# Kernel tuning notes

Measured on AMD Instinct MI355X. Metric: run time of the kernel, lower is better.

The kernel has to match this reference:

```python
import jax, jax.numpy as jnp
import numpy as np

B, T, F = 256, 192, 8
CARD0, CARD1 = 1000, 100
E0, E1 = 32, 16
H = 512
D_IN = F + E0 + E1  # 56


def _glorot(key, shape):
    fan_in, fan_out = shape[0], shape[-1]
    lim = jnp.sqrt(6.0 / (fan_in + fan_out))
    return jax.random.uniform(key, shape, jnp.float32, -lim, lim)


def setup_inputs() -> dict:
    key = jax.random.key(0)
    ks = jax.random.split(key, 16)
    return {
        "x_cont": jax.random.normal(ks[0], (B, T, F), jnp.float32),
        "cat0": jax.random.randint(ks[1], (B, T), 0, CARD0),
        "cat1": jax.random.randint(ks[2], (B, T), 0, CARD1),
        "emb0": _glorot(ks[3], (CARD0, E0)),
        "emb1": _glorot(ks[4], (CARD1, E1)),
        "Wk1": _glorot(ks[5], (D_IN, 4 * H)),
        "Wr1": _glorot(ks[6], (H, 4 * H)),
        "b1": jnp.zeros((4 * H,), jnp.float32).at[H:2 * H].set(1.0),  # unit_forget_bias
        "Wk2": _glorot(ks[7], (H, 4 * H)),
        "Wr2": _glorot(ks[8], (H, 4 * H)),
        "b2": jnp.zeros((4 * H,), jnp.float32).at[H:2 * H].set(1.0),
        "Wmu": _glorot(ks[9], (H, 1)),
        "bmu": _glorot(ks[10], (1, 1))[0],
        "Wsig": _glorot(ks[11], (H, 1)),
        "bsig": _glorot(ks[12], (1, 1))[0],
    }


def _lstm(x, Wk, Wr, b):
    # x: [B, T, D]; Keras gate order i, f, g(c), o; zero initial states (inference mode,
    # dropout/recurrent_dropout inactive when training=False).
    xz = jnp.einsum('btd,dk->btk', x, Wk) + b  # precompute input projection for all steps
    h0 = jnp.zeros((x.shape[0], H), x.dtype)

    def step(carry, z_t):
        h, c = carry
        z = z_t + h @ Wr  # [B, 4H]
        i, f, g, o = jnp.split(z, 4, axis=-1)
        i = jax.nn.sigmoid(i)
        f = jax.nn.sigmoid(f)
        g = jnp.tanh(g)
        o = jax.nn.sigmoid(o)
        c = f * c + i * g
        h = o * jnp.tanh(c)
        return (h, c), h

    _, hs = jax.lax.scan(step, (h0, h0), jnp.swapaxes(xz, 0, 1))  # [T, B, H]
    return jnp.swapaxes(hs, 0, 1)


def reference(x_cont, cat0, cat1, emb0, emb1, Wk1, Wr1, b1, Wk2, Wr2, b2, Wmu, bmu, Wsig, bsig):
    x = jnp.concatenate([x_cont, emb0[cat0], emb1[cat1]], axis=-1)  # [B, T, 56]
    x = _lstm(x, Wk1, Wr1, b1)
    x = _lstm(x, Wk2, Wr2, b2)
    mu = x @ Wmu + bmu                      # count_data=False -> raw mu
    sigma = jax.nn.softplus(x @ Wsig + bsig)
    return (mu, sigma)
```

## Files before the change

kernel.cpp:

```cpp
#include <hip/hip_runtime.h>
#include <math.h>

#define Bsz 256
#define Tsz 192
#define Fc 8
#define E0c 32
#define E1c 16
#define Hc 512
#define G4 2048
#define DINP 64
#define K1t 576
#define K2t 1024
#define NBLK 256
#define LBLK 32
#define KPAD1 584
#define KPAD2 1032
#define LDSB_BYTES (64 * KPAD2 * 2)
#define SLOT_STRIDE 16

typedef __attribute__((ext_vector_type(8))) short short8;
typedef __attribute__((ext_vector_type(4))) float f32x4;

template<int N> struct IC { static constexpr int v = N; };
template<int C, int CMAX, typename F>
__device__ __forceinline__ void static_for(F&& f) {
    if constexpr (C < CMAX) {
        f(IC<C>{});
        static_for<C + 1, CMAX>(f);
    }
}

static __device__ __forceinline__ float bf2f(ushort u) {
    return __uint_as_float(((uint)u) << 16);
}
static __device__ __forceinline__ ushort f2bf(float f) {
    uint u = __float_as_uint(f);
    u = (u + 0x7fffu + ((u >> 16) & 1u)) >> 16;
    return (ushort)u;
}

static __device__ __forceinline__ uint poll_sc1(const uint* p) {
    uint v;
    asm volatile("global_load_dword %0, %1, off sc1\n\t"
                 "s_waitcnt vmcnt(0)"
                 : "=v"(v) : "v"((unsigned long long)p) : "memory");
    return v;
}
static __device__ __forceinline__ void store_slot_sc1(uint* p, uint v) {
    asm volatile("global_store_dword %0, %1, off sc1"
                 :: "v"((unsigned long long)p), "v"(v) : "memory");
}

__global__ __launch_bounds__(256) void build_x_kernel(
    const float* __restrict__ x_cont, const int* __restrict__ cat0,
    const int* __restrict__ cat1, const float* __restrict__ emb0,
    const float* __restrict__ emb1, ushort* __restrict__ x_bf)
{
    int idx = blockIdx.x * 256 + threadIdx.x;
    if (idx >= Tsz * Bsz * DINP) return;
    int d = idx & 63;
    int row = idx >> 6;
    int t = row >> 8;
    int b = row & 255;
    float v = 0.f;
    if (d < Fc)                  v = x_cont[(b * Tsz + t) * Fc + d];
    else if (d < Fc + E0c)       v = emb0[cat0[b * Tsz + t] * E0c + (d - Fc)];
    else if (d < Fc + E0c + E1c) v = emb1[cat1[b * Tsz + t] * E1c + (d - Fc - E0c)];
    x_bf[idx] = f2bf(v);
}

__global__ __launch_bounds__(256) void transpose_w_kernel(
    const float* __restrict__ in, ushort* __restrict__ out, int K, int ldout, int coff)
{
    __shared__ float tile[32][33];
    int k0 = blockIdx.x * 32;
    int n0 = blockIdx.y * 32;
    int tx = threadIdx.x & 31, ty = threadIdx.x >> 5;
    #pragma unroll
    for (int p = 0; p < 4; ++p) {
        int k = k0 + ty + p * 8;
        tile[ty + p * 8][tx] = (k < K) ? in[k * G4 + n0 + tx] : 0.f;
    }
    __syncthreads();
    #pragma unroll
    for (int p = 0; p < 4; ++p) {
        int nl = ty + p * 8;
        out[(size_t)(n0 + nl) * ldout + coff + k0 + tx] = f2bf(tile[tx][nl]);
    }
}

static __device__ __forceinline__ void wait_slots(const uint* arr, uint tg) {
    const uint* p = arr + (threadIdx.x & 31) * SLOT_STRIDE;
    while (true) {
        uint v = poll_sc1(p);
        if (__all((int)(v >= tg))) break;
        __builtin_amdgcn_s_sleep(1);
    }
}

template<int KS_IN, int KS_TOT, int LDA_IN, int KPADv, bool HAS_DEP>
static __device__ __forceinline__ void run_layer(
    const ushort* __restrict__ Ain,
    ushort* __restrict__ hbuf,
    const ushort* __restrict__ hz,
    const ushort* __restrict__ Wt,
    const float* __restrict__ bias,
    ushort* B_lds,
    const uint* dep_slots,
    uint* own_slots, uint* my_slot,
    int m0, int j0)
{
    constexpr int KS_R = KS_TOT - KS_IN;
    constexpr int KL = KS_TOT * 32;
    constexpr int SEGS = KL / 8;
    int tid = threadIdx.x;
    int lane = tid & 63, wv = tid >> 6;
    int lane15 = lane & 15, quad = lane >> 4;

    for (int i = tid; i < 64 * SEGS; i += 256) {
        int row = i / SEGS, seg = i - row * SEGS;
        int gz = (row >> 4) * Hc + j0 + (row & 15);
        *(uint4*)&B_lds[row * KPADv + seg * 8] =
            *(const uint4*)(Wt + (size_t)gz * KL + seg * 8);
    }
    __syncthreads();

    float bgate[4];
    #pragma unroll
    for (int gt = 0; gt < 4; ++gt) bgate[gt] = bias[gt * Hc + j0 + lane15];
    float cst[4] = {0.f, 0.f, 0.f, 0.f};

    int arow = m0 + wv * 16 + lane15;
    int crow0 = m0 + wv * 16 + quad * 4;

    for (int t = 0; t < Tsz; ++t) {
        f32x4 acc[4];
        #pragma unroll
        for (int gt = 0; gt < 4; ++gt) acc[gt] = (f32x4){0.f, 0.f, 0.f, 0.f};

        if constexpr (HAS_DEP) {
            if (tid < 64) wait_slots(dep_slots, (uint)(t + 1));
            __syncthreads();
        }
        {
            const ushort* p0 = Ain + ((size_t)t * Bsz + arow) * LDA_IN + quad * 8;
            uint4 bufA[KS_IN];
            static_for<0, KS_IN>([&](auto Kc) {
                constexpr int ks = decltype(Kc)::v;
                bufA[ks] = *(const uint4*)(p0 + ks * 32);
            });
            asm volatile("" ::: "memory");
            static_for<0, KS_IN>([&](auto Kc) {
                constexpr int ks = decltype(Kc)::v;
                short8 av = __builtin_bit_cast(short8, bufA[ks]);
                #pragma unroll
                for (int gt = 0; gt < 4; ++gt) {
                    short8 bfr = *(const short8*)&B_lds[(gt * 16 + lane15) * KPADv + ks * 32 + quad * 8];
                    acc[gt] = __builtin_amdgcn_mfma_f32_16x16x32_bf16(av, bfr, acc[gt], 0, 0, 0);
                }
            });
        }

        if (t) {
            if (tid < 64) wait_slots(own_slots, (uint)t);
            __syncthreads();
        }
        {
            const ushort* p1base = (t > 0) ? (hbuf + (size_t)(t - 1) * Bsz * Hc) : hz;
            const ushort* p1 = p1base + (size_t)arow * Hc + quad * 8;
            uint4 bufB[KS_R];
            static_for<0, KS_R>([&](auto Kc) {
                constexpr int ks = decltype(Kc)::v;
                bufB[ks] = *(const uint4*)(p1 + ks * 32);
            });
            asm volatile("" ::: "memory");
            static_for<0, KS_R>([&](auto Kc) {
                constexpr int ks = decltype(Kc)::v;
                short8 av = __builtin_bit_cast(short8, bufB[ks]);
                #pragma unroll
                for (int gt = 0; gt < 4; ++gt) {
                    short8 bfr = *(const short8*)&B_lds[(gt * 16 + lane15) * KPADv + (KS_IN + ks) * 32 + quad * 8];
                    acc[gt] = __builtin_amdgcn_mfma_f32_16x16x32_bf16(av, bfr, acc[gt], 0, 0, 0);
                }
            });
        }

        uint hv[4];
        #pragma unroll
        for (int r = 0; r < 4; ++r) {
            float zi = acc[0][r] + bgate[0];
            float zf = acc[1][r] + bgate[1];
            float zg = acc[2][r] + bgate[2];
            float zo = acc[3][r] + bgate[3];
            float ig = 1.f / (1.f + __expf(-zi));
            float fg = 1.f / (1.f + __expf(-zf));
            float gg = tanhf(zg);
            float og = 1.f / (1.f + __expf(-zo));
            float cn = fg * cst[r] + ig * gg;
            cst[r] = cn;
            float hn = og * tanhf(cn);
            hv[r] = (uint)f2bf(hn);
        }
        {
            unsigned long long hb = (unsigned long long)
                &hbuf[((size_t)t * Bsz + crow0) * Hc + j0 + lane15];
            asm volatile(
                "global_store_short %0, %1, off sc1\n\t"
                "global_store_short %0, %2, off offset:1024 sc1\n\t"
                "global_store_short %0, %3, off offset:2048 sc1\n\t"
                "global_store_short %0, %4, off offset:3072 sc1\n\t"
                "s_waitcnt vmcnt(0)"
                :: "v"(hb), "v"(hv[0]), "v"(hv[1]), "v"(hv[2]), "v"(hv[3])
                : "memory");
        }

        __syncthreads();
        if (tid == 0)
            store_slot_sc1(my_slot, (uint)(t + 1));
    }
}

__global__ __launch_bounds__(256, 1) void deepar_persistent(
    const ushort* __restrict__ x_bf,
    const ushort* __restrict__ Wt1, const ushort* __restrict__ Wt2,
    const float* __restrict__ b1, const float* __restrict__ b2,
    ushort* __restrict__ h1, ushort* __restrict__ h2,
    const ushort* __restrict__ hz,
    const float* __restrict__ Wmu, const float* __restrict__ bmu,
    const float* __restrict__ Wsig, const float* __restrict__ bsig,
    float* __restrict__ out, uint* __restrict__ slots)
{
    extern __shared__ ushort B_lds[];

    int bid = blockIdx.x;
    int xcd = bid & 7;
    int g = xcd >> 1;
    int role = xcd & 1;
    int jb = bid >> 3;
    int m0 = g * 64;
    int j0 = jb * 16;
    uint* s_l1 = slots + (g * 2 + 0) * LBLK * SLOT_STRIDE;
    uint* s_l2 = slots + (g * 2 + 1) * LBLK * SLOT_STRIDE;

    if (role == 0) {
        run_layer<2, 18, DINP, KPAD1, false>(x_bf, h1, hz, Wt1, b1, B_lds,
                                             nullptr, s_l1, s_l1 + jb * SLOT_STRIDE, m0, j0);
        return;
    }
    run_layer<16, 32, Hc, KPAD2, true>(h1, h2, hz, Wt2, b2, B_lds,
                                       s_l1, s_l2, s_l2 + jb * SLOT_STRIDE, m0, j0);

    if (threadIdx.x < 64) wait_slots(s_l2, (uint)Tsz);
    __syncthreads();

    int lane = threadIdx.x & 63, wv = threadIdx.x >> 6;
    float wm[8], wsg[8];
    #pragma unroll
    for (int i = 0; i < 8; ++i) {
        wm[i] = Wmu[lane * 8 + i];
        wsg[i] = Wsig[lane * 8 + i];
    }
    float bmu0 = bmu[0], bsg0 = bsig[0];
    for (int i = jb * 4 + wv; i < 64 * Tsz; i += 128) {
        int b = m0 + (i & 63);
        int t = i >> 6;
        const ushort* hp = h2 + ((size_t)t * Bsz + b) * Hc + lane * 8;
        short8 hvv = *(const short8*)hp;
        float smu = 0.f, ssg = 0.f;
        #pragma unroll
        for (int e = 0; e < 8; ++e) {
            float f = bf2f((ushort)hvv[e]);
            smu += f * wm[e];
            ssg += f * wsg[e];
        }
        #pragma unroll
        for (int off = 32; off > 0; off >>= 1) {
            smu += __shfl_down(smu, off, 64);
            ssg += __shfl_down(ssg, off, 64);
        }
        if (lane == 0) {
            int oi = b * Tsz + t;
            float sg = ssg + bsg0;
            float sp = sg > 0.f ? sg + log1pf(__expf(-sg)) : log1pf(__expf(sg));
            out[oi] = smu + bmu0;
            out[Bsz * Tsz + oi] = sp;
        }
    }
}

extern "C" void kernel_launch(void* const* d_in, const int* in_sizes, int n_in,
                              void* d_out, int out_size, void* d_ws, size_t ws_size,
                              hipStream_t stream) {
    const float* x_cont = (const float*)d_in[0];
    const int*   cat0   = (const int*)d_in[1];
    const int*   cat1   = (const int*)d_in[2];
    const float* emb0   = (const float*)d_in[3];
    const float* emb1   = (const float*)d_in[4];
    const float* Wk1    = (const float*)d_in[5];
    const float* Wr1    = (const float*)d_in[6];
    const float* b1     = (const float*)d_in[7];
    const float* Wk2    = (const float*)d_in[8];
    const float* Wr2    = (const float*)d_in[9];
    const float* b2     = (const float*)d_in[10];
    const float* Wmu    = (const float*)d_in[11];
    const float* bmu    = (const float*)d_in[12];
    const float* Wsig   = (const float*)d_in[13];
    const float* bsig   = (const float*)d_in[14];
    float* out = (float*)d_out;

    const size_t slots_bytes = 8 * LBLK * SLOT_STRIDE * 4;

    char* ws = (char*)d_ws;
    uint*   slots = (uint*)ws;                                 ws += slots_bytes;
    ushort* x_bf  = (ushort*)ws;                               ws += (size_t)Tsz * Bsz * DINP * 2;
    ushort* Wt1   = (ushort*)ws;                               ws += (size_t)G4 * K1t * 2;
    ushort* Wt2   = (ushort*)ws;                               ws += (size_t)G4 * K2t * 2;
    ushort* h1    = (ushort*)ws;                               ws += (size_t)Tsz * Bsz * Hc * 2;
    ushort* h2    = (ushort*)ws;                               ws += (size_t)Tsz * Bsz * Hc * 2;
    ushort* hz    = (ushort*)ws;                               ws += (size_t)Bsz * Hc * 2;

    hipMemsetAsync(slots, 0, slots_bytes, stream);
    hipMemsetAsync(hz, 0, (size_t)Bsz * Hc * 2, stream);

    build_x_kernel<<<(Tsz * Bsz * DINP + 255) / 256, 256, 0, stream>>>(
        x_cont, cat0, cat1, emb0, emb1, x_bf);
    transpose_w_kernel<<<dim3(2, 64), 256, 0, stream>>>(Wk1, Wt1, 56, K1t, 0);
    transpose_w_kernel<<<dim3(16, 64), 256, 0, stream>>>(Wr1, Wt1, Hc, K1t, DINP);
    transpose_w_kernel<<<dim3(16, 64), 256, 0, stream>>>(Wk2, Wt2, Hc, K2t, 0);
    transpose_w_kernel<<<dim3(16, 64), 256, 0, stream>>>(Wr2, Wt2, Hc, K2t, Hc);

    hipFuncSetAttribute((const void*)deepar_persistent,
                        hipFuncAttributeMaxDynamicSharedMemorySize, LDSB_BYTES);
    deepar_persistent<<<dim3(NBLK), dim3(256), LDSB_BYTES, stream>>>(
        x_bf, Wt1, Wt2, b1, b2, h1, h2, hz, Wmu, bmu, Wsig, bsig, out, slots);
}
```

Baseline: 1.371 ms.

## Replace per-block slot flags with atomic counters and cache recurrent weights in registers

The per-block slot arrays polled with a wave vote are replaced by a single atomic counter per group/layer, bumped once per step and spun on with one address. The bump is deferred until just before the next step's recurrent read, so the input-projection MFMAs overlap the store drain. Recurrent weight fragments are hoisted from LDS into registers once per layer. The t=0 zero-h buffer read is skipped, and sigmoid/tanh use fast rcp-based forms. Together these cut per-step sync latency and LDS traffic, at the cost of much higher register pressure (wB for layer 2 is 4x16 short8) and a busy-spin without sleep.

```diff
diff --git a/kernel.cpp b/kernel.cpp
--- a/kernel.cpp
+++ b/kernel.cpp
@@ -12,11 +12,10 @@
 #define K1t 576
 #define K2t 1024
 #define NBLK 256
-#define LBLK 32
 #define KPAD1 584
 #define KPAD2 1032
 #define LDSB_BYTES (64 * KPAD2 * 2)
-#define SLOT_STRIDE 16
+#define CTR_STRIDE 64
 
 typedef __attribute__((ext_vector_type(8))) short short8;
 typedef __attribute__((ext_vector_type(4))) float f32x4;
@@ -39,6 +38,13 @@
     return (ushort)u;
 }
 
+static __device__ __forceinline__ float sigm_f(float x) {
+    return __builtin_amdgcn_rcpf(1.f + __expf(-x));
+}
+static __device__ __forceinline__ float tanh_f(float x) {
+    return 1.f - 2.f * __builtin_amdgcn_rcpf(1.f + __expf(2.f * x));
+}
+
 static __device__ __forceinline__ uint poll_sc1(const uint* p) {
     uint v;
     asm volatile("global_load_dword %0, %1, off sc1\n\t"
@@ -46,9 +52,12 @@
                  : "=v"(v) : "v"((unsigned long long)p) : "memory");
     return v;
 }
-static __device__ __forceinline__ void store_slot_sc1(uint* p, uint v) {
-    asm volatile("global_store_dword %0, %1, off sc1"
-                 :: "v"((unsigned long long)p), "v"(v) : "memory");
+static __device__ __forceinline__ void bump_sc1(uint* p) {
+    asm volatile("global_atomic_add %0, %1, off sc1"
+                 :: "v"((unsigned long long)p), "v"(1u) : "memory");
+}
+static __device__ __forceinline__ void wait_ge(const uint* p, uint tgt) {
+    while (poll_sc1(p) < tgt) {}
 }
 
 __global__ __launch_bounds__(256) void build_x_kernel(
@@ -89,25 +98,15 @@
     }
 }
 
-static __device__ __forceinline__ void wait_slots(const uint* arr, uint tg) {
-    const uint* p = arr + (threadIdx.x & 31) * SLOT_STRIDE;
-    while (true) {
-        uint v = poll_sc1(p);
-        if (__all((int)(v >= tg))) break;
-        __builtin_amdgcn_s_sleep(1);
-    }
-}
-
 template<int KS_IN, int KS_TOT, int LDA_IN, int KPADv, bool HAS_DEP>
 static __device__ __forceinline__ void run_layer(
     const ushort* __restrict__ Ain,
     ushort* __restrict__ hbuf,
-    const ushort* __restrict__ hz,
     const ushort* __restrict__ Wt,
     const float* __restrict__ bias,
     ushort* B_lds,
-    const uint* dep_slots,
-    uint* own_slots, uint* my_slot,
+    const uint* dep_ctr,
+    uint* own_ctr,
     int m0, int j0)
 {
     constexpr int KS_R = KS_TOT - KS_IN;
@@ -125,6 +124,15 @@
     }
     __syncthreads();
 
+    short8 wB[4][KS_R];
+    static_for<0, KS_R>([&](auto Kc) {
+        constexpr int ks = decltype(Kc)::v;
+        #pragma unroll
+        for (int gt = 0; gt < 4; ++gt)
+            wB[gt][ks] = *(const short8*)&B_lds[(gt * 16 + lane15) * KPADv
+                                               + (KS_IN + ks) * 32 + quad * 8];
+    });
+
     float bgate[4];
     #pragma unroll
     for (int gt = 0; gt < 4; ++gt) bgate[gt] = bias[gt * Hc + j0 + lane15];
@@ -134,40 +142,45 @@
     int crow0 = m0 + wv * 16 + quad * 4;
 
     for (int t = 0; t < Tsz; ++t) {
+        if constexpr (HAS_DEP) {
+            if (tid < 64) wait_ge(dep_ctr, 32u * (uint)(t + 1));
+            __syncthreads();
+        }
         f32x4 acc[4];
         #pragma unroll
         for (int gt = 0; gt < 4; ++gt) acc[gt] = (f32x4){0.f, 0.f, 0.f, 0.f};
-
-        if constexpr (HAS_DEP) {
-            if (tid < 64) wait_slots(dep_slots, (uint)(t + 1));
-            __syncthreads();
-        }
         {
             const ushort* p0 = Ain + ((size_t)t * Bsz + arow) * LDA_IN + quad * 8;
-            uint4 bufA[KS_IN];
-            static_for<0, KS_IN>([&](auto Kc) {
-                constexpr int ks = decltype(Kc)::v;
-                bufA[ks] = *(const uint4*)(p0 + ks * 32);
+            constexpr int CHA = (KS_IN < 8) ? KS_IN : 8;
+            static_for<0, KS_IN / CHA>([&](auto Cc) {
+                constexpr int c0 = decltype(Cc)::v * CHA;
+                uint4 bufA[CHA];
+                static_for<0, CHA>([&](auto Kc) {
+                    constexpr int ks = decltype(Kc)::v;
+                    bufA[ks] = *(const uint4*)(p0 + (c0 + ks) * 32);
+                });
+                asm volatile("" ::: "memory");
+                static_for<0, CHA>([&](auto Kc) {
+                    constexpr int ks = decltype(Kc)::v;
+                    short8 av = __builtin_bit_cast(short8, bufA[ks]);
+                    #pragma unroll
+                    for (int gt = 0; gt < 4; ++gt) {
+                        short8 bfr = *(const short8*)&B_lds[(gt * 16 + lane15) * KPADv
+                                                           + (c0 + ks) * 32 + quad * 8];
+                        acc[gt] = __builtin_amdgcn_mfma_f32_16x16x32_bf16(av, bfr, acc[gt], 0, 0, 0);
+                    }
+                });
             });
-            asm volatile("" ::: "memory");
-            static_for<0, KS_IN>([&](auto Kc) {
-                constexpr int ks = decltype(Kc)::v;
-                short8 av = __builtin_bit_cast(short8, bufA[ks]);
-                #pragma unroll
-                for (int gt = 0; gt < 4; ++gt) {
-                    short8 bfr = *(const short8*)&B_lds[(gt * 16 + lane15) * KPADv + ks * 32 + quad * 8];
-                    acc[gt] = __builtin_amdgcn_mfma_f32_16x16x32_bf16(av, bfr, acc[gt], 0, 0, 0);
-                }
-            });
         }
 
         if (t) {
-            if (tid < 64) wait_slots(own_slots, (uint)t);
+            asm volatile("s_waitcnt vmcnt(0)" ::: "memory");
             __syncthreads();
-        }
-        {
-            const ushort* p1base = (t > 0) ? (hbuf + (size_t)(t - 1) * Bsz * Hc) : hz;
-            const ushort* p1 = p1base + (size_t)arow * Hc + quad * 8;
+            if (tid == 0) bump_sc1(own_ctr);
+            if (tid < 64) wait_ge(own_ctr, 32u * (uint)t);
+            __syncthreads();
+
+            const ushort* p1 = hbuf + ((size_t)(t - 1) * Bsz + arow) * Hc + quad * 8;
             uint4 bufB[KS_R];
             static_for<0, KS_R>([&](auto Kc) {
                 constexpr int ks = decltype(Kc)::v;
@@ -178,10 +191,8 @@
                 constexpr int ks = decltype(Kc)::v;
                 short8 av = __builtin_bit_cast(short8, bufB[ks]);
                 #pragma unroll
-                for (int gt = 0; gt < 4; ++gt) {
-                    short8 bfr = *(const short8*)&B_lds[(gt * 16 + lane15) * KPADv + (KS_IN + ks) * 32 + quad * 8];
-                    acc[gt] = __builtin_amdgcn_mfma_f32_16x16x32_bf16(av, bfr, acc[gt], 0, 0, 0);
-                }
+                for (int gt = 0; gt < 4; ++gt)
+                    acc[gt] = __builtin_amdgcn_mfma_f32_16x16x32_bf16(av, wB[gt][ks], acc[gt], 0, 0, 0);
             });
         }
 
@@ -192,13 +203,13 @@
             float zf = acc[1][r] + bgate[1];
             float zg = acc[2][r] + bgate[2];
             float zo = acc[3][r] + bgate[3];
-            float ig = 1.f / (1.f + __expf(-zi));
-            float fg = 1.f / (1.f + __expf(-zf));
-            float gg = tanhf(zg);
-            float og = 1.f / (1.f + __expf(-zo));
+            float ig = sigm_f(zi);
+            float fg = sigm_f(zf);
+            float gg = tanh_f(zg);
+            float og = sigm_f(zo);
             float cn = fg * cst[r] + ig * gg;
             cst[r] = cn;
-            float hn = og * tanhf(cn);
+            float hn = og * tanh_f(cn);
             hv[r] = (uint)f2bf(hn);
         }
         {
@@ -208,16 +219,14 @@
                 "global_store_short %0, %1, off sc1\n\t"
                 "global_store_short %0, %2, off offset:1024 sc1\n\t"
                 "global_store_short %0, %3, off offset:2048 sc1\n\t"
-                "global_store_short %0, %4, off offset:3072 sc1\n\t"
-                "s_waitcnt vmcnt(0)"
+                "global_store_short %0, %4, off offset:3072 sc1"
                 :: "v"(hb), "v"(hv[0]), "v"(hv[1]), "v"(hv[2]), "v"(hv[3])
                 : "memory");
         }
-
-        __syncthreads();
-        if (tid == 0)
-            store_slot_sc1(my_slot, (uint)(t + 1));
-    }
+    }
+    asm volatile("s_waitcnt vmcnt(0)" ::: "memory");
+    __syncthreads();
+    if (tid == 0) bump_sc1(own_ctr);
 }
 
 __global__ __launch_bounds__(256, 1) void deepar_persistent(
@@ -225,10 +234,9 @@
     const ushort* __restrict__ Wt1, const ushort* __restrict__ Wt2,
     const float* __restrict__ b1, const float* __restrict__ b2,
     ushort* __restrict__ h1, ushort* __restrict__ h2,
-    const ushort* __restrict__ hz,
     const float* __restrict__ Wmu, const float* __restrict__ bmu,
     const float* __restrict__ Wsig, const float* __restrict__ bsig,
-    float* __restrict__ out, uint* __restrict__ slots)
+    float* __restrict__ out, uint* __restrict__ ctrs)
 {
     extern __shared__ ushort B_lds[];
 
@@ -239,18 +247,18 @@
     int jb = bid >> 3;
     int m0 = g * 64;
     int j0 = jb * 16;
-    uint* s_l1 = slots + (g * 2 + 0) * LBLK * SLOT_STRIDE;
-    uint* s_l2 = slots + (g * 2 + 1) * LBLK * SLOT_STRIDE;
+    uint* c1 = ctrs + (g * 2 + 0) * CTR_STRIDE;
+    uint* c2 = ctrs + (g * 2 + 1) * CTR_STRIDE;
 
     if (role == 0) {
-        run_layer<2, 18, DINP, KPAD1, false>(x_bf, h1, hz, Wt1, b1, B_lds,
-                                             nullptr, s_l1, s_l1 + jb * SLOT_STRIDE, m0, j0);
+        run_layer<2, 18, DINP, KPAD1, false>(x_bf, h1, Wt1, b1, B_lds,
+                                             nullptr, c1, m0, j0);
         return;
     }
-    run_layer<16, 32, Hc, KPAD2, true>(h1, h2, hz, Wt2, b2, B_lds,
-                                       s_l1, s_l2, s_l2 + jb * SLOT_STRIDE, m0, j0);
-
-    if (threadIdx.x < 64) wait_slots(s_l2, (uint)Tsz);
+    run_layer<16, 32, Hc, KPAD2, true>(h1, h2, Wt2, b2, B_lds,
+                                       c1, c2, m0, j0);
+
+    if (threadIdx.x < 64) wait_ge(c2, 32u * (uint)Tsz);
     __syncthreads();
 
     int lane = threadIdx.x & 63, wv = threadIdx.x >> 6;
@@ -308,19 +316,17 @@
     const float* bsig   = (const float*)d_in[14];
     float* out = (float*)d_out;
 
-    const size_t slots_bytes = 8 * LBLK * SLOT_STRIDE * 4;
+    const size_t ctrs_bytes = 8 * CTR_STRIDE * 4;
 
     char* ws = (char*)d_ws;
-    uint*   slots = (uint*)ws;                                 ws += slots_bytes;
+    uint*   ctrs  = (uint*)ws;                                 ws += ctrs_bytes;
     ushort* x_bf  = (ushort*)ws;                               ws += (size_t)Tsz * Bsz * DINP * 2;
     ushort* Wt1   = (ushort*)ws;                               ws += (size_t)G4 * K1t * 2;
     ushort* Wt2   = (ushort*)ws;                               ws += (size_t)G4 * K2t * 2;
     ushort* h1    = (ushort*)ws;                               ws += (size_t)Tsz * Bsz * Hc * 2;
     ushort* h2    = (ushort*)ws;                               ws += (size_t)Tsz * Bsz * Hc * 2;
-    ushort* hz    = (ushort*)ws;                               ws += (size_t)Bsz * Hc * 2;
-
-    hipMemsetAsync(slots, 0, slots_bytes, stream);
-    hipMemsetAsync(hz, 0, (size_t)Bsz * Hc * 2, stream);
+
+    hipMemsetAsync(ctrs, 0, ctrs_bytes, stream);
 
     build_x_kernel<<<(Tsz * Bsz * DINP + 255) / 256, 256, 0, stream>>>(
         x_cont, cat0, cat1, emb0, emb1, x_bf);
@@ -332,5 +338,5 @@
     hipFuncSetAttribute((const void*)deepar_persistent,
                         hipFuncAttributeMaxDynamicSharedMemorySize, LDSB_BYTES);
     deepar_persistent<<<dim3(NBLK), dim3(256), LDSB_BYTES, stream>>>(
-        x_bf, Wt1, Wt2, b1, b2, h1, h2, hz, Wmu, bmu, Wsig, bsig, out, slots);
-}
+        x_bf, Wt1, Wt2, b1, b2, h1, h2, Wmu, bmu, Wsig, bsig, out, ctrs);
+}
```

Measured after the change: 1.729 ms. 26.2% more time.

## Push per-consumer progress flags instead of polling shared slot arrays

Applied to the files above, without the earlier changes.

Each producer block now writes its step counter into a private flag array owned by each consumer block (64 stores for layer 1, covering same-layer peers and layer-2 consumers; 32 for layer 2). Consumers poll only their own contiguous flag region. The intent is to reduce cross-XCD contention and coherence traffic on shared polled cache lines in the recurrent barrier. It costs more flag stores per step. It also adds a watchdog that breaks out of the spin wait after a fixed number of iterations, which could let a block proceed without its dependency being satisfied.

```diff
diff --git a/kernel.cpp b/kernel.cpp
--- a/kernel.cpp
+++ b/kernel.cpp
@@ -17,6 +17,9 @@
 #define KPAD2 1032
 #define LDSB_BYTES (64 * KPAD2 * 2)
 #define SLOT_STRIDE 16
+#define DEP_OFF (32 * SLOT_STRIDE)
+#define PF_BLOCK (64 * SLOT_STRIDE)
+#define WD_WAIT (1 << 17)
 
 typedef __attribute__((ext_vector_type(8))) short short8;
 typedef __attribute__((ext_vector_type(4))) float f32x4;
@@ -91,14 +94,16 @@
 
 static __device__ __forceinline__ void wait_slots(const uint* arr, uint tg) {
     const uint* p = arr + (threadIdx.x & 31) * SLOT_STRIDE;
+    int it = 0;
     while (true) {
         uint v = poll_sc1(p);
         if (__all((int)(v >= tg))) break;
+        if (++it >= WD_WAIT) break;
         __builtin_amdgcn_s_sleep(1);
     }
 }
 
-template<int KS_IN, int KS_TOT, int LDA_IN, int KPADv, bool HAS_DEP>
+template<int KS_IN, int KS_TOT, int LDA_IN, int KPADv, bool HAS_DEP, int FANOUT>
 static __device__ __forceinline__ void run_layer(
     const ushort* __restrict__ Ain,
     ushort* __restrict__ hbuf,
@@ -106,9 +111,8 @@
     const ushort* __restrict__ Wt,
     const float* __restrict__ bias,
     ushort* B_lds,
-    const uint* dep_slots,
-    uint* own_slots, uint* my_slot,
-    int m0, int j0)
+    uint* pflags,
+    int g, int jb, int m0, int j0)
 {
     constexpr int KS_R = KS_TOT - KS_IN;
     constexpr int KL = KS_TOT * 32;
@@ -116,6 +120,19 @@
     int tid = threadIdx.x;
     int lane = tid & 63, wv = tid >> 6;
     int lane15 = lane & 15, quad = lane >> 4;
+    int bid = jb * 8 + g * 2 + (HAS_DEP ? 1 : 0);
+
+    const uint* own_arr = pflags + bid * PF_BLOCK;
+    const uint* dep_arr = own_arr + DEP_OFF;
+
+    uint* pub_dst = nullptr;
+    if (tid < FANOUT) {
+        int j = tid & 31;
+        int cons_role = (HAS_DEP ? 1 : (tid >> 5));
+        int cons_bid = j * 8 + g * 2 + cons_role;
+        pub_dst = pflags + cons_bid * PF_BLOCK + ((tid >> 5) ? DEP_OFF : 0)
+                + jb * SLOT_STRIDE;
+    }
 
     for (int i = tid; i < 64 * SEGS; i += 256) {
         int row = i / SEGS, seg = i - row * SEGS;
@@ -139,7 +156,7 @@
         for (int gt = 0; gt < 4; ++gt) acc[gt] = (f32x4){0.f, 0.f, 0.f, 0.f};
 
         if constexpr (HAS_DEP) {
-            if (tid < 64) wait_slots(dep_slots, (uint)(t + 1));
+            if (tid < 64) wait_slots(dep_arr, (uint)(t + 1));
             __syncthreads();
         }
         {
@@ -162,7 +179,7 @@
         }
 
         if (t) {
-            if (tid < 64) wait_slots(own_slots, (uint)t);
+            if (tid < 64) wait_slots(own_arr, (uint)t);
             __syncthreads();
         }
         {
@@ -215,8 +232,8 @@
         }
 
         __syncthreads();
-        if (tid == 0)
-            store_slot_sc1(my_slot, (uint)(t + 1));
+        if (tid < FANOUT)
+            store_slot_sc1(pub_dst, (uint)(t + 1));
     }
 }
 
@@ -228,7 +245,7 @@
     const ushort* __restrict__ hz,
     const float* __restrict__ Wmu, const float* __restrict__ bmu,
     const float* __restrict__ Wsig, const float* __restrict__ bsig,
-    float* __restrict__ out, uint* __restrict__ slots)
+    float* __restrict__ out, uint* __restrict__ pflags)
 {
     extern __shared__ ushort B_lds[];
 
@@ -239,18 +256,17 @@
     int jb = bid >> 3;
     int m0 = g * 64;
     int j0 = jb * 16;
-    uint* s_l1 = slots + (g * 2 + 0) * LBLK * SLOT_STRIDE;
-    uint* s_l2 = slots + (g * 2 + 1) * LBLK * SLOT_STRIDE;
 
     if (role == 0) {
-        run_layer<2, 18, DINP, KPAD1, false>(x_bf, h1, hz, Wt1, b1, B_lds,
-                                             nullptr, s_l1, s_l1 + jb * SLOT_STRIDE, m0, j0);
+        run_layer<2, 18, DINP, KPAD1, false, 64>(x_bf, h1, hz, Wt1, b1, B_lds,
+                                                 pflags, g, jb, m0, j0);
         return;
     }
-    run_layer<16, 32, Hc, KPAD2, true>(h1, h2, hz, Wt2, b2, B_lds,
-                                       s_l1, s_l2, s_l2 + jb * SLOT_STRIDE, m0, j0);
-
-    if (threadIdx.x < 64) wait_slots(s_l2, (uint)Tsz);
+    run_layer<16, 32, Hc, KPAD2, true, 32>(h1, h2, hz, Wt2, b2, B_lds,
+                                           pflags, g, jb, m0, j0);
+
+    const uint* own_arr = pflags + bid * PF_BLOCK;
+    if (threadIdx.x < 64) wait_slots(own_arr, (uint)Tsz);
     __syncthreads();
 
     int lane = threadIdx.x & 63, wv = threadIdx.x >> 6;
@@ -308,10 +324,10 @@
     const float* bsig   = (const float*)d_in[14];
     float* out = (float*)d_out;
 
-    const size_t slots_bytes = 8 * LBLK * SLOT_STRIDE * 4;
+    const size_t pflags_bytes = (size_t)NBLK * PF_BLOCK * 4;
 
     char* ws = (char*)d_ws;
-    uint*   slots = (uint*)ws;                                 ws += slots_bytes;
+    uint*   pflags = (uint*)ws;                                ws += pflags_bytes;
     ushort* x_bf  = (ushort*)ws;                               ws += (size_t)Tsz * Bsz * DINP * 2;
     ushort* Wt1   = (ushort*)ws;                               ws += (size_t)G4 * K1t * 2;
     ushort* Wt2   = (ushort*)ws;                               ws += (size_t)G4 * K2t * 2;
@@ -319,7 +335,7 @@
     ushort* h2    = (ushort*)ws;                               ws += (size_t)Tsz * Bsz * Hc * 2;
     ushort* hz    = (ushort*)ws;                               ws += (size_t)Bsz * Hc * 2;
 
-    hipMemsetAsync(slots, 0, slots_bytes, stream);
+    hipMemsetAsync(pflags, 0, pflags_bytes, stream);
     hipMemsetAsync(hz, 0, (size_t)Bsz * Hc * 2, stream);
 
     build_x_kernel<<<(Tsz * Bsz * DINP + 255) / 256, 256, 0, stream>>>(
@@ -332,5 +348,5 @@
     hipFuncSetAttribute((const void*)deepar_persistent,
                         hipFuncAttributeMaxDynamicSharedMemorySize, LDSB_BYTES);
     deepar_persistent<<<dim3(NBLK), dim3(256), LDSB_BYTES, stream>>>(
-        x_bf, Wt1, Wt2, b1, b2, h1, h2, hz, Wmu, bmu, Wsig, bsig, out, slots);
-}
+        x_bf, Wt1, Wt2, b1, b2, h1, h2, hz, Wmu, bmu, Wsig, bsig, out, pflags);
+}
```

After: 1.360 ms. Within noise of the previous version (-0.8%).
